# Performance work log

Measured on AMD Instinct MI355X. Metric: run time of the kernel, lower is better.

Reference implementation:

```python
import math
import jax, jax.numpy as jnp
import numpy as np

B, S, HID, NH = 4, 1024, 768, 12
D = HID // NH
R_ACT = 0.5
R_ATTN = 0.5


def act_prune_mask(a, ratio):
    # per-sample kth-smallest magnitude threshold (torch.kthvalue on flatten(1))
    n = int(np.prod(a.shape[1:]))
    k = int(np.clip(n * ratio, 1, n))
    mag = jnp.abs(a)
    thr = jnp.sort(mag.reshape(a.shape[0], -1), axis=1)[:, k - 1]
    thr = thr.reshape((a.shape[0],) + (1,) * (a.ndim - 1))
    return mag >= thr


def setup_inputs() -> dict:
    key = jax.random.key(0)
    ks = jax.random.split(key, 5)
    inp = {
        "hidden_states": jax.random.normal(ks[0], (B, S, HID), dtype=jnp.float32),
        "Wq": jax.random.normal(ks[1], (HID, HID), dtype=jnp.float32) * 0.02,
        "bq": jnp.zeros((HID,), dtype=jnp.float32),
        "Wk": jax.random.normal(ks[2], (HID, HID), dtype=jnp.float32) * 0.02,
        "bk": jnp.zeros((HID,), dtype=jnp.float32),
        "Wv": jax.random.normal(ks[3], (HID, HID), dtype=jnp.float32) * 0.02,
        "bv": jnp.zeros((HID,), dtype=jnp.float32),
        "Wo": jax.random.normal(ks[4], (HID, HID), dtype=jnp.float32) * 0.02,
        "bo": jnp.zeros((HID,), dtype=jnp.float32),
    }
    return inp


def reference(hidden_states, Wq, bq, Wk, bk, Wv, bv, Wo, bo):
    b, s, hid = hidden_states.shape

    # prune mask on input activations (saved for backward in the original; forward math unchanged)
    mask_h = act_prune_mask(hidden_states, R_ACT)
    _hs_prune = jnp.where(mask_h, hidden_states, 0.0)

    q = jnp.matmul(hidden_states, Wq.T) + bq
    k = jnp.matmul(hidden_states, Wk.T) + bk
    v = jnp.matmul(hidden_states, Wv.T) + bv

    def split_heads(x):
        return x.reshape(b, s, NH, D).transpose(0, 2, 1, 3)  # [B,H,S,D]

    q4, k4, v4 = split_heads(q), split_heads(k), split_heads(v)

    mask_q = act_prune_mask(q4, R_ACT)
    mask_k = act_prune_mask(k4, R_ACT)
    _qp = jnp.where(mask_q, q4, 0.0)
    _kp = jnp.where(mask_k, k4, 0.0)

    scores = jnp.einsum("bhqd,bhkd->bhqk", q4, k4) / math.sqrt(D)
    probs = jax.nn.softmax(scores, axis=-1)

    mask_p = act_prune_mask(probs, R_ATTN)
    _pp = jnp.where(mask_p, probs, 0.0)
    mask_v = act_prune_mask(v4, R_ACT)
    _vp = jnp.where(mask_v, v4, 0.0)

    ctx = jnp.einsum("bhqk,bhkd->bhqd", probs, v4)
    ctx = ctx.transpose(0, 2, 1, 3).reshape(b, s, hid)

    mask_c = act_prune_mask(ctx, R_ACT)
    _cp = jnp.where(mask_c, ctx, 0.0)

    out = jnp.matmul(ctx, Wo.T) + bo  # proj_dropout rate = 0.0 (identity)
    return (out, probs)  # vis=True -> weights = attention_probs
```

## Files before the change

kernel.cpp:

```cpp
#include <hip/hip_runtime.h>
#include <hip/hip_bf16.h>

typedef __attribute__((ext_vector_type(4))) float f32x4;
typedef __attribute__((ext_vector_type(8))) short bf16x8;
typedef __attribute__((ext_vector_type(4))) int i32x4;

#define SEQ 1024
#define HIDV 768
#define NH 12
#define HD 64
#define QBLK 64

static __device__ __forceinline__ unsigned short f2b(float f) {
  unsigned u = __builtin_bit_cast(unsigned, f);
  u = (u + 0x7fffu + ((u >> 16) & 1u)) >> 16;
  return (unsigned short)u;
}

static __device__ __forceinline__ void gl16(const unsigned short* g, unsigned short* l) {
  __builtin_amdgcn_global_load_lds(
      (const __attribute__((address_space(1))) unsigned int*)g,
      (__attribute__((address_space(3))) unsigned int*)l, 16, 0, 0);
}

static __device__ __forceinline__ void bar_lgkm() {
  asm volatile("s_waitcnt lgkmcnt(0)" ::: "memory");
  __builtin_amdgcn_sched_barrier(0);
  __builtin_amdgcn_s_barrier();
  __builtin_amdgcn_sched_barrier(0);
}

__global__ __launch_bounds__(256) void convert_all(
    const float* __restrict__ X, const float* __restrict__ Wq,
    const float* __restrict__ Wk, const float* __restrict__ Wv,
    const float* __restrict__ Wo, unsigned short* __restrict__ dst) {
  long i = (long)blockIdx.x * 256 + threadIdx.x;
  const long N4 = (3145728L + 4 * 589824L) / 4;
  if (i >= N4) return;
  long e = i * 4;
  const float* src; long off;
  if (e < 3145728L)      { src = X;  off = e; }
  else if (e < 3735552L) { src = Wq; off = e - 3145728L; }
  else if (e < 4325376L) { src = Wk; off = e - 3735552L; }
  else if (e < 4915200L) { src = Wv; off = e - 4325376L; }
  else                   { src = Wo; off = e - 4915200L; }
  const float4 v = *reinterpret_cast<const float4*>(src + off);
  ushort4 o;
  o.x = f2b(v.x); o.y = f2b(v.y); o.z = f2b(v.z); o.w = f2b(v.w);
  *reinterpret_cast<ushort4*>(dst + e) = o;
}

__global__ __launch_bounds__(256) void qkv_gemm(
    const unsigned short* __restrict__ Xb,
    const unsigned short* __restrict__ Wqb, const unsigned short* __restrict__ Wkb,
    const unsigned short* __restrict__ Wvb,
    const float* __restrict__ bq, const float* __restrict__ bk, const float* __restrict__ bv,
    unsigned short* __restrict__ Qh, unsigned short* __restrict__ Kh,
    unsigned short* __restrict__ VT) {
  __shared__ __align__(16) unsigned short la[2][128 * 32];
  __shared__ __align__(16) unsigned short lb[2][128 * 32];
  const int z = blockIdx.z;
  const unsigned short* Wb = (z == 0) ? Wqb : (z == 1) ? Wkb : Wvb;
  const float* bias = (z == 0) ? bq : (z == 1) ? bk : bv;
  const int m0 = blockIdx.x * 128, n0 = blockIdx.y * 128;
  const int tid = threadIdx.x;
  const int wave = tid >> 6, lane = tid & 63, g = lane >> 4, c = lane & 15;
  const int wr = (wave >> 1) * 64, wc = (wave & 1) * 64;

  const int sr = wave * 16 + (lane >> 2);
  const int scol = (lane & 3) * 8;
  const unsigned short* Ag = &Xb[(size_t)(m0 + sr) * HIDV + scol];
  const unsigned short* Bg = &Wb[(size_t)(n0 + sr) * HIDV + scol];

  gl16(Ag, &la[0][(wave * 16) * 32]);
  gl16(Ag + (size_t)64 * HIDV, &la[0][(64 + wave * 16) * 32]);
  gl16(Bg, &lb[0][(wave * 16) * 32]);
  gl16(Bg + (size_t)64 * HIDV, &lb[0][(64 + wave * 16) * 32]);
  __syncthreads();

  f32x4 acc[4][4] = {};
  for (int t = 0; t < 24; t++) {
    const int cur = t & 1;
    if (t < 23) {
      const int kt = (t + 1) * 32;
      gl16(Ag + kt, &la[cur ^ 1][(wave * 16) * 32]);
      gl16(Ag + (size_t)64 * HIDV + kt, &la[cur ^ 1][(64 + wave * 16) * 32]);
      gl16(Bg + kt, &lb[cur ^ 1][(wave * 16) * 32]);
      gl16(Bg + (size_t)64 * HIDV + kt, &lb[cur ^ 1][(64 + wave * 16) * 32]);
    }
    bf16x8 af[4], bfr[4];
#pragma unroll
    for (int m = 0; m < 4; m++)
      af[m] = *reinterpret_cast<bf16x8*>(&la[cur][(wr + m * 16 + c) * 32 + g * 8]);
#pragma unroll
    for (int n = 0; n < 4; n++)
      bfr[n] = *reinterpret_cast<bf16x8*>(&lb[cur][(wc + n * 16 + c) * 32 + g * 8]);
#pragma unroll
    for (int m = 0; m < 4; m++)
#pragma unroll
      for (int n = 0; n < 4; n++)
        acc[m][n] = __builtin_amdgcn_mfma_f32_16x16x32_bf16(af[m], bfr[n], acc[m][n], 0, 0, 0);
    __syncthreads();
  }
  float bv4[4];
#pragma unroll
  for (int n = 0; n < 4; n++) bv4[n] = bias[n0 + wc + n * 16 + c];
  if (z < 2) {
    unsigned short* dst = (z == 0) ? Qh : Kh;
#pragma unroll
    for (int m = 0; m < 4; m++) {
      int rb_ = m0 + wr + m * 16 + g * 4;
#pragma unroll
      for (int n = 0; n < 4; n++) {
        int col = n0 + wc + n * 16 + c;
        int h = col >> 6, d = col & 63;
#pragma unroll
        for (int r = 0; r < 4; r++) {
          int row = rb_ + r;
          int b = row >> 10, s = row & 1023;
          dst[((size_t)(b * NH + h) * SEQ + s) * HD + d] = f2b(acc[m][n][r] + bv4[n]);
        }
      }
    }
  } else {
#pragma unroll
    for (int m = 0; m < 4; m++) {
      int rb_ = m0 + wr + m * 16 + g * 4;
      int b = rb_ >> 10, s = rb_ & 1023;
#pragma unroll
      for (int n = 0; n < 4; n++) {
        int col = n0 + wc + n * 16 + c;
        int h = col >> 6, d = col & 63;
        ushort4 o;
        o.x = f2b(acc[m][n][0] + bv4[n]);
        o.y = f2b(acc[m][n][1] + bv4[n]);
        o.z = f2b(acc[m][n][2] + bv4[n]);
        o.w = f2b(acc[m][n][3] + bv4[n]);
        *reinterpret_cast<ushort4*>(&VT[((size_t)(b * NH + h) * HD + d) * SEQ + s]) = o;
      }
    }
  }
}

#define EXPC 0.18033688f
__global__ __launch_bounds__(256) void attn_fused(
    const unsigned short* __restrict__ Qh, const unsigned short* __restrict__ Kh,
    const unsigned short* __restrict__ VT,
    float* __restrict__ probs, unsigned short* __restrict__ CTX) {
  __shared__ __align__(16) unsigned short ldsk[2][64 * 72];
  __shared__ __align__(16) unsigned short ldsv[2][64 * 72];
  __shared__ __align__(16) unsigned short lp[64 * 72];
  const int lin = blockIdx.x;
  const int swz = (lin & 7) * 96 + (lin >> 3);
  const int bh = swz >> 4, rb = (swz & 15) * QBLK;
  const int b = bh / NH, h = bh - b * NH;
  const unsigned short* Qp = Qh + (size_t)bh * SEQ * HD;
  const unsigned short* Kp = Kh + (size_t)bh * SEQ * HD;
  const unsigned short* Vp = VT + (size_t)bh * HD * SEQ;
  float* P = probs + (size_t)bh * SEQ * SEQ;
  const int tid = threadIdx.x, wave = tid >> 6, lane = tid & 63, g = lane >> 4, c = lane & 15;
  const int wrow = wave * 16;
  const int str = tid >> 3;
  const int stc = (tid & 7) * 8;

  bf16x8 aq[2];
#pragma unroll
  for (int ks = 0; ks < 2; ks++)
    aq[ks] = *reinterpret_cast<const bf16x8*>(&Qp[(size_t)(rb + wrow + c) * HD + ks * 32 + g * 8]);

  i32x4 kr0, kr1, vr0, vr1;
  kr0 = *reinterpret_cast<const i32x4*>(&Kp[(size_t)str * HD + stc]);
  kr1 = *reinterpret_cast<const i32x4*>(&Kp[(size_t)(str + 32) * HD + stc]);
  *reinterpret_cast<i32x4*>(&ldsk[0][str * 72 + stc]) = kr0;
  *reinterpret_cast<i32x4*>(&ldsk[0][(str + 32) * 72 + stc]) = kr1;
  bar_lgkm();

  float lsum = 0.f;
  for (int ct = 0; ct < 16; ct++) {
    const int cur = ct & 1;
    if (ct < 15) {
      kr0 = *reinterpret_cast<const i32x4*>(&Kp[(size_t)((ct + 1) * 64 + str) * HD + stc]);
      kr1 = *reinterpret_cast<const i32x4*>(&Kp[(size_t)((ct + 1) * 64 + str + 32) * HD + stc]);
    }
    f32x4 sreg[4] = {};
    __builtin_amdgcn_s_setprio(1);
#pragma unroll
    for (int ks = 0; ks < 2; ks++) {
      bf16x8 kf[4];
#pragma unroll
      for (int kb = 0; kb < 4; kb++)
        kf[kb] = *reinterpret_cast<bf16x8*>(&ldsk[cur][(kb * 16 + c) * 72 + ks * 32 + g * 8]);
#pragma unroll
      for (int kb = 0; kb < 4; kb++)
        sreg[kb] = __builtin_amdgcn_mfma_f32_16x16x32_bf16(kf[kb], aq[ks], sreg[kb], 0, 0, 0);
    }
    __builtin_amdgcn_s_setprio(0);
#pragma unroll
    for (int kb = 0; kb < 4; kb++)
#pragma unroll
      for (int r = 0; r < 4; r++)
        lsum += __builtin_amdgcn_exp2f(sreg[kb][r] * EXPC);
    if (ct < 15) {
      *reinterpret_cast<i32x4*>(&ldsk[cur ^ 1][str * 72 + stc]) = kr0;
      *reinterpret_cast<i32x4*>(&ldsk[cur ^ 1][(str + 32) * 72 + stc]) = kr1;
      bar_lgkm();
    }
  }
  float s = lsum;
  s += __shfl_xor(s, 16);
  s += __shfl_xor(s, 32);
  const float linv = 1.f / s;

  kr0 = *reinterpret_cast<const i32x4*>(&Kp[(size_t)str * HD + stc]);
  kr1 = *reinterpret_cast<const i32x4*>(&Kp[(size_t)(str + 32) * HD + stc]);
  vr0 = *reinterpret_cast<const i32x4*>(&Vp[(size_t)str * SEQ + stc]);
  vr1 = *reinterpret_cast<const i32x4*>(&Vp[(size_t)(str + 32) * SEQ + stc]);
  *reinterpret_cast<i32x4*>(&ldsk[0][str * 72 + stc]) = kr0;
  *reinterpret_cast<i32x4*>(&ldsk[0][(str + 32) * 72 + stc]) = kr1;
  *reinterpret_cast<i32x4*>(&ldsv[0][str * 72 + stc]) = vr0;
  *reinterpret_cast<i32x4*>(&ldsv[0][(str + 32) * 72 + stc]) = vr1;
  bar_lgkm();

  f32x4 acc[4] = {};
  for (int ct = 0; ct < 16; ct++) {
    const int cur = ct & 1;
    if (ct < 15) {
      kr0 = *reinterpret_cast<const i32x4*>(&Kp[(size_t)((ct + 1) * 64 + str) * HD + stc]);
      kr1 = *reinterpret_cast<const i32x4*>(&Kp[(size_t)((ct + 1) * 64 + str + 32) * HD + stc]);
      vr0 = *reinterpret_cast<const i32x4*>(&Vp[(size_t)str * SEQ + (ct + 1) * 64 + stc]);
      vr1 = *reinterpret_cast<const i32x4*>(&Vp[(size_t)(str + 32) * SEQ + (ct + 1) * 64 + stc]);
    }
    f32x4 sreg[4] = {};
    __builtin_amdgcn_s_setprio(1);
#pragma unroll
    for (int ks = 0; ks < 2; ks++) {
      bf16x8 kf[4];
#pragma unroll
      for (int kb = 0; kb < 4; kb++)
        kf[kb] = *reinterpret_cast<bf16x8*>(&ldsk[cur][(kb * 16 + c) * 72 + ks * 32 + g * 8]);
#pragma unroll
      for (int kb = 0; kb < 4; kb++)
        sreg[kb] = __builtin_amdgcn_mfma_f32_16x16x32_bf16(kf[kb], aq[ks], sreg[kb], 0, 0, 0);
    }
    __builtin_amdgcn_s_setprio(0);
    {
      float* Prow = &P[(size_t)(rb + wrow + c) * SEQ + ct * 64];
#pragma unroll
      for (int kb = 0; kb < 4; kb++) {
        f32x4 p;
#pragma unroll
        for (int r = 0; r < 4; r++)
          p[r] = __builtin_amdgcn_exp2f(sreg[kb][r] * EXPC) * linv;
        *reinterpret_cast<f32x4*>(&Prow[kb * 16 + g * 4]) = p;
        uint2 pk;
        pk.x = (unsigned)f2b(p[0]) | ((unsigned)f2b(p[1]) << 16);
        pk.y = (unsigned)f2b(p[2]) | ((unsigned)f2b(p[3]) << 16);
        *reinterpret_cast<uint2*>(&lp[(wrow + c) * 72 + kb * 16 + g * 4]) = pk;
      }
    }
    __builtin_amdgcn_s_setprio(1);
#pragma unroll
    for (int ks = 0; ks < 2; ks++) {
      bf16x8 pa, vf[4];
      pa = *reinterpret_cast<bf16x8*>(&lp[(wrow + c) * 72 + ks * 32 + g * 8]);
#pragma unroll
      for (int db = 0; db < 4; db++)
        vf[db] = *reinterpret_cast<bf16x8*>(&ldsv[cur][(db * 16 + c) * 72 + ks * 32 + g * 8]);
#pragma unroll
      for (int db = 0; db < 4; db++)
        acc[db] = __builtin_amdgcn_mfma_f32_16x16x32_bf16(pa, vf[db], acc[db], 0, 0, 0);
    }
    __builtin_amdgcn_s_setprio(0);
    if (ct < 15) {
      *reinterpret_cast<i32x4*>(&ldsk[cur ^ 1][str * 72 + stc]) = kr0;
      *reinterpret_cast<i32x4*>(&ldsk[cur ^ 1][(str + 32) * 72 + stc]) = kr1;
      *reinterpret_cast<i32x4*>(&ldsv[cur ^ 1][str * 72 + stc]) = vr0;
      *reinterpret_cast<i32x4*>(&ldsv[cur ^ 1][(str + 32) * 72 + stc]) = vr1;
      bar_lgkm();
    }
  }

  bar_lgkm();
#pragma unroll
  for (int db = 0; db < 4; db++)
#pragma unroll
    for (int r = 0; r < 4; r++)
      lp[(wrow + g * 4 + r) * 72 + db * 16 + c] = f2b(acc[db][r]);
  bar_lgkm();
  {
    const int q = tid >> 2, seg = (tid & 3) * 16;
    const unsigned short* src = &lp[q * 72 + seg];
    unsigned short* dst = &CTX[(size_t)(b * SEQ + rb + q) * HIDV + h * HD + seg];
    i32x4 t0 = *reinterpret_cast<const i32x4*>(&src[0]);
    i32x4 t1 = *reinterpret_cast<const i32x4*>(&src[8]);
    *reinterpret_cast<i32x4*>(&dst[0]) = t0;
    *reinterpret_cast<i32x4*>(&dst[8]) = t1;
  }
}

__global__ __launch_bounds__(256) void proj_gemm(
    const unsigned short* __restrict__ Ab, const unsigned short* __restrict__ Wb,
    const float* __restrict__ bias, float* __restrict__ out) {
  __shared__ __align__(16) unsigned short la[2][64 * 32];
  __shared__ __align__(16) unsigned short lb[2][128 * 32];
  const int m0 = blockIdx.x * 64, n0 = blockIdx.y * 128;
  const int tid = threadIdx.x;
  const int wave = tid >> 6, lane = tid & 63, g = lane >> 4, c = lane & 15;
  const int wr = (wave >> 1) * 32, wc = (wave & 1) * 64;
  const int srb = wave * 16 + (lane >> 2);
  const int scol = (lane & 3) * 8;
  const unsigned short* Ag = &Ab[(size_t)(m0 + srb) * HIDV + scol];
  const unsigned short* Bg = &Wb[(size_t)(n0 + srb) * HIDV + scol];

#define PROJ_STAGE(buf, kt)                                               \
  do {                                                                    \
    gl16(Ag + (kt), &la[buf][(wave * 16) * 32]);                          \
    gl16(Bg + (kt), &lb[buf][(wave * 16) * 32]);                          \
    gl16(Bg + (size_t)64 * HIDV + (kt), &lb[buf][(64 + wave * 16) * 32]); \
  } while (0)

  PROJ_STAGE(0, 0);
  __syncthreads();

  f32x4 acc[2][4] = {};
  for (int t = 0; t < 24; t++) {
    const int cur = t & 1;
    if (t < 23) PROJ_STAGE(cur ^ 1, (t + 1) * 32);
    bf16x8 af[2], bfr[4];
#pragma unroll
    for (int m = 0; m < 2; m++)
      af[m] = *reinterpret_cast<bf16x8*>(&la[cur][(wr + m * 16 + c) * 32 + g * 8]);
#pragma unroll
    for (int n = 0; n < 4; n++)
      bfr[n] = *reinterpret_cast<bf16x8*>(&lb[cur][(wc + n * 16 + c) * 32 + g * 8]);
#pragma unroll
    for (int m = 0; m < 2; m++)
#pragma unroll
      for (int n = 0; n < 4; n++)
        acc[m][n] = __builtin_amdgcn_mfma_f32_16x16x32_bf16(af[m], bfr[n], acc[m][n], 0, 0, 0);
    __syncthreads();
  }
#undef PROJ_STAGE
  float bv4[4];
#pragma unroll
  for (int n = 0; n < 4; n++) bv4[n] = bias[n0 + wc + n * 16 + c];
#pragma unroll
  for (int m = 0; m < 2; m++) {
    int rb_ = m0 + wr + m * 16 + g * 4;
#pragma unroll
    for (int n = 0; n < 4; n++) {
      int col = n0 + wc + n * 16 + c;
#pragma unroll
      for (int r = 0; r < 4; r++)
        out[(size_t)(rb_ + r) * HIDV + col] = acc[m][n][r] + bv4[n];
    }
  }
}

extern "C" void kernel_launch(void* const* d_in, const int* in_sizes, int n_in,
                              void* d_out, int out_size, void* d_ws, size_t ws_size,
                              hipStream_t stream) {
  const float* X  = (const float*)d_in[0];
  const float* Wq = (const float*)d_in[1];
  const float* bq = (const float*)d_in[2];
  const float* Wk = (const float*)d_in[3];
  const float* bk = (const float*)d_in[4];
  const float* Wv = (const float*)d_in[5];
  const float* bv = (const float*)d_in[6];
  const float* Wo = (const float*)d_in[7];
  const float* bo = (const float*)d_in[8];
  float* out = (float*)d_out;
  float* probs = out + 3145728;

  unsigned short* Xb  = (unsigned short*)d_ws;
  unsigned short* Wqb = Xb + 3145728;
  unsigned short* Wkb = Wqb + 589824;
  unsigned short* Wvb = Wkb + 589824;
  unsigned short* Wob = Wvb + 589824;
  unsigned short* Qh  = Wob + 589824;
  unsigned short* Kh  = Qh + 3145728;
  unsigned short* VT  = Kh + 3145728;
  unsigned short* CTX = VT + 3145728;

  convert_all<<<5376, 256, 0, stream>>>(X, Wq, Wk, Wv, Wo, Xb);
  qkv_gemm<<<dim3(32, 6, 3), 256, 0, stream>>>(Xb, Wqb, Wkb, Wvb, bq, bk, bv, Qh, Kh, VT);
  attn_fused<<<dim3(768), 256, 0, stream>>>(Qh, Kh, VT, probs, CTX);
  proj_gemm<<<dim3(64, 6), 256, 0, stream>>>(CTX, Wob, bo, out);
}
```

Before: 105.8 us.

## Make attention single-pass by staging unnormalized bf16 exp scores in LDS

The attention kernel no longer runs a separate QK^T pass just to compute softmax row sums. It computes exp scores once and keeps them unnormalized as bf16 in a large dynamic LDS buffer covering the full 64x1024 score tile. It accumulates row sums alongside, then scales both the context output and the stored scores by 1/sum, writing probs to global memory in coalesced rows at the end. In exchange, LDS use grows to roughly 150 KB per block, K/V staging loses its double buffering, and probs are now rounded through bf16 before being written as fp32.

Result: slower. 165.5 us (+56.3%).

```diff
diff --git a/kernel.cpp b/kernel.cpp
--- a/kernel.cpp
+++ b/kernel.cpp
@@ -10,12 +10,17 @@
 #define NH 12
 #define HD 64
 #define QBLK 64
+#define SPITCH 1032
+#define ATTN_LDS ((64 * SPITCH + 2 * 64 * 72) * 2)
 
 static __device__ __forceinline__ unsigned short f2b(float f) {
   unsigned u = __builtin_bit_cast(unsigned, f);
   u = (u + 0x7fffu + ((u >> 16) & 1u)) >> 16;
   return (unsigned short)u;
 }
+static __device__ __forceinline__ float b2f(unsigned short u) {
+  return __builtin_bit_cast(float, (unsigned)u << 16);
+}
 
 static __device__ __forceinline__ void gl16(const unsigned short* g, unsigned short* l) {
   __builtin_amdgcn_global_load_lds(
@@ -25,6 +30,11 @@
 
 static __device__ __forceinline__ void bar_lgkm() {
   asm volatile("s_waitcnt lgkmcnt(0)" ::: "memory");
+  __builtin_amdgcn_sched_barrier(0);
+  __builtin_amdgcn_s_barrier();
+  __builtin_amdgcn_sched_barrier(0);
+}
+static __device__ __forceinline__ void bar_only() {
   __builtin_amdgcn_sched_barrier(0);
   __builtin_amdgcn_s_barrier();
   __builtin_amdgcn_sched_barrier(0);
@@ -147,9 +157,12 @@
     const unsigned short* __restrict__ Qh, const unsigned short* __restrict__ Kh,
     const unsigned short* __restrict__ VT,
     float* __restrict__ probs, unsigned short* __restrict__ CTX) {
-  __shared__ __align__(16) unsigned short ldsk[2][64 * 72];
-  __shared__ __align__(16) unsigned short ldsv[2][64 * 72];
-  __shared__ __align__(16) unsigned short lp[64 * 72];
+  extern __shared__ __align__(16) unsigned short smem[];
+  unsigned short* Sbuf = smem;
+  unsigned short* ldsk = smem + 64 * SPITCH;
+  unsigned short* ldsv = ldsk + 64 * 72;
+  float* linvf = (float*)ldsv;
+
   const int lin = blockIdx.x;
   const int swz = (lin & 7) * 96 + (lin >> 3);
   const int bh = swz >> 4, rb = (swz & 15) * QBLK;
@@ -171,59 +184,17 @@
   i32x4 kr0, kr1, vr0, vr1;
   kr0 = *reinterpret_cast<const i32x4*>(&Kp[(size_t)str * HD + stc]);
   kr1 = *reinterpret_cast<const i32x4*>(&Kp[(size_t)(str + 32) * HD + stc]);
-  *reinterpret_cast<i32x4*>(&ldsk[0][str * 72 + stc]) = kr0;
-  *reinterpret_cast<i32x4*>(&ldsk[0][(str + 32) * 72 + stc]) = kr1;
-  bar_lgkm();
-
-  float lsum = 0.f;
-  for (int ct = 0; ct < 16; ct++) {
-    const int cur = ct & 1;
-    if (ct < 15) {
-      kr0 = *reinterpret_cast<const i32x4*>(&Kp[(size_t)((ct + 1) * 64 + str) * HD + stc]);
-      kr1 = *reinterpret_cast<const i32x4*>(&Kp[(size_t)((ct + 1) * 64 + str + 32) * HD + stc]);
-    }
-    f32x4 sreg[4] = {};
-    __builtin_amdgcn_s_setprio(1);
-#pragma unroll
-    for (int ks = 0; ks < 2; ks++) {
-      bf16x8 kf[4];
-#pragma unroll
-      for (int kb = 0; kb < 4; kb++)
-        kf[kb] = *reinterpret_cast<bf16x8*>(&ldsk[cur][(kb * 16 + c) * 72 + ks * 32 + g * 8]);
-#pragma unroll
-      for (int kb = 0; kb < 4; kb++)
-        sreg[kb] = __builtin_amdgcn_mfma_f32_16x16x32_bf16(kf[kb], aq[ks], sreg[kb], 0, 0, 0);
-    }
-    __builtin_amdgcn_s_setprio(0);
-#pragma unroll
-    for (int kb = 0; kb < 4; kb++)
-#pragma unroll
-      for (int r = 0; r < 4; r++)
-        lsum += __builtin_amdgcn_exp2f(sreg[kb][r] * EXPC);
-    if (ct < 15) {
-      *reinterpret_cast<i32x4*>(&ldsk[cur ^ 1][str * 72 + stc]) = kr0;
-      *reinterpret_cast<i32x4*>(&ldsk[cur ^ 1][(str + 32) * 72 + stc]) = kr1;
-      bar_lgkm();
-    }
-  }
-  float s = lsum;
-  s += __shfl_xor(s, 16);
-  s += __shfl_xor(s, 32);
-  const float linv = 1.f / s;
-
-  kr0 = *reinterpret_cast<const i32x4*>(&Kp[(size_t)str * HD + stc]);
-  kr1 = *reinterpret_cast<const i32x4*>(&Kp[(size_t)(str + 32) * HD + stc]);
   vr0 = *reinterpret_cast<const i32x4*>(&Vp[(size_t)str * SEQ + stc]);
   vr1 = *reinterpret_cast<const i32x4*>(&Vp[(size_t)(str + 32) * SEQ + stc]);
-  *reinterpret_cast<i32x4*>(&ldsk[0][str * 72 + stc]) = kr0;
-  *reinterpret_cast<i32x4*>(&ldsk[0][(str + 32) * 72 + stc]) = kr1;
-  *reinterpret_cast<i32x4*>(&ldsv[0][str * 72 + stc]) = vr0;
-  *reinterpret_cast<i32x4*>(&ldsv[0][(str + 32) * 72 + stc]) = vr1;
+  *reinterpret_cast<i32x4*>(&ldsk[str * 72 + stc]) = kr0;
+  *reinterpret_cast<i32x4*>(&ldsk[(str + 32) * 72 + stc]) = kr1;
+  *reinterpret_cast<i32x4*>(&ldsv[str * 72 + stc]) = vr0;
+  *reinterpret_cast<i32x4*>(&ldsv[(str + 32) * 72 + stc]) = vr1;
   bar_lgkm();
 
+  float lsum = 0.f;
   f32x4 acc[4] = {};
   for (int ct = 0; ct < 16; ct++) {
-    const int cur = ct & 1;
     if (ct < 15) {
       kr0 = *reinterpret_cast<const i32x4*>(&Kp[(size_t)((ct + 1) * 64 + str) * HD + stc]);
       kr1 = *reinterpret_cast<const i32x4*>(&Kp[(size_t)((ct + 1) * 64 + str + 32) * HD + stc]);
@@ -237,64 +208,87 @@
       bf16x8 kf[4];
 #pragma unroll
       for (int kb = 0; kb < 4; kb++)
-        kf[kb] = *reinterpret_cast<bf16x8*>(&ldsk[cur][(kb * 16 + c) * 72 + ks * 32 + g * 8]);
+        kf[kb] = *reinterpret_cast<bf16x8*>(&ldsk[(kb * 16 + c) * 72 + ks * 32 + g * 8]);
 #pragma unroll
       for (int kb = 0; kb < 4; kb++)
         sreg[kb] = __builtin_amdgcn_mfma_f32_16x16x32_bf16(kf[kb], aq[ks], sreg[kb], 0, 0, 0);
     }
     __builtin_amdgcn_s_setprio(0);
     {
-      float* Prow = &P[(size_t)(rb + wrow + c) * SEQ + ct * 64];
+      unsigned short* srow = &Sbuf[(wrow + c) * SPITCH + ct * 64];
 #pragma unroll
       for (int kb = 0; kb < 4; kb++) {
         f32x4 p;
 #pragma unroll
-        for (int r = 0; r < 4; r++)
-          p[r] = __builtin_amdgcn_exp2f(sreg[kb][r] * EXPC) * linv;
-        *reinterpret_cast<f32x4*>(&Prow[kb * 16 + g * 4]) = p;
+        for (int r = 0; r < 4; r++) {
+          p[r] = __builtin_amdgcn_exp2f(sreg[kb][r] * EXPC);
+          lsum += p[r];
+        }
         uint2 pk;
         pk.x = (unsigned)f2b(p[0]) | ((unsigned)f2b(p[1]) << 16);
         pk.y = (unsigned)f2b(p[2]) | ((unsigned)f2b(p[3]) << 16);
-        *reinterpret_cast<uint2*>(&lp[(wrow + c) * 72 + kb * 16 + g * 4]) = pk;
+        *reinterpret_cast<uint2*>(&srow[kb * 16 + g * 4]) = pk;
       }
     }
     __builtin_amdgcn_s_setprio(1);
 #pragma unroll
     for (int ks = 0; ks < 2; ks++) {
       bf16x8 pa, vf[4];
-      pa = *reinterpret_cast<bf16x8*>(&lp[(wrow + c) * 72 + ks * 32 + g * 8]);
+      pa = *reinterpret_cast<bf16x8*>(&Sbuf[(wrow + c) * SPITCH + ct * 64 + ks * 32 + g * 8]);
 #pragma unroll
       for (int db = 0; db < 4; db++)
-        vf[db] = *reinterpret_cast<bf16x8*>(&ldsv[cur][(db * 16 + c) * 72 + ks * 32 + g * 8]);
+        vf[db] = *reinterpret_cast<bf16x8*>(&ldsv[(db * 16 + c) * 72 + ks * 32 + g * 8]);
 #pragma unroll
       for (int db = 0; db < 4; db++)
         acc[db] = __builtin_amdgcn_mfma_f32_16x16x32_bf16(pa, vf[db], acc[db], 0, 0, 0);
     }
     __builtin_amdgcn_s_setprio(0);
     if (ct < 15) {
-      *reinterpret_cast<i32x4*>(&ldsk[cur ^ 1][str * 72 + stc]) = kr0;
-      *reinterpret_cast<i32x4*>(&ldsk[cur ^ 1][(str + 32) * 72 + stc]) = kr1;
-      *reinterpret_cast<i32x4*>(&ldsv[cur ^ 1][str * 72 + stc]) = vr0;
-      *reinterpret_cast<i32x4*>(&ldsv[cur ^ 1][(str + 32) * 72 + stc]) = vr1;
+      bar_only();
+      *reinterpret_cast<i32x4*>(&ldsk[str * 72 + stc]) = kr0;
+      *reinterpret_cast<i32x4*>(&ldsk[(str + 32) * 72 + stc]) = kr1;
+      *reinterpret_cast<i32x4*>(&ldsv[str * 72 + stc]) = vr0;
+      *reinterpret_cast<i32x4*>(&ldsv[(str + 32) * 72 + stc]) = vr1;
       bar_lgkm();
     }
   }
 
-  bar_lgkm();
+  float s = lsum;
+  s += __shfl_xor(s, 16);
+  s += __shfl_xor(s, 32);
+  const float linv = 1.f / s;
+  bar_only();
+  if (lane < 16) linvf[wrow + lane] = linv;
+
+  float lv[4];
+#pragma unroll
+  for (int r = 0; r < 4; r++) lv[r] = linvf[wrow + g * 4 + r];
 #pragma unroll
   for (int db = 0; db < 4; db++)
 #pragma unroll
     for (int r = 0; r < 4; r++)
-      lp[(wrow + g * 4 + r) * 72 + db * 16 + c] = f2b(acc[db][r]);
+      ldsk[(wrow + g * 4 + r) * 72 + db * 16 + c] = f2b(acc[db][r] * lv[r]);
   bar_lgkm();
   {
     const int q = tid >> 2, seg = (tid & 3) * 16;
-    const unsigned short* src = &lp[q * 72 + seg];
+    const unsigned short* src = &ldsk[q * 72 + seg];
     unsigned short* dst = &CTX[(size_t)(b * SEQ + rb + q) * HIDV + h * HD + seg];
     i32x4 t0 = *reinterpret_cast<const i32x4*>(&src[0]);
     i32x4 t1 = *reinterpret_cast<const i32x4*>(&src[8]);
     *reinterpret_cast<i32x4*>(&dst[0]) = t0;
     *reinterpret_cast<i32x4*>(&dst[8]) = t1;
+  }
+
+#pragma unroll 4
+  for (int r = 0; r < 64; r++) {
+    const float lr = linvf[r];
+    uint2 pk = *reinterpret_cast<const uint2*>(&Sbuf[r * SPITCH + tid * 4]);
+    float4 o;
+    o.x = b2f((unsigned short)(pk.x & 0xffff)) * lr;
+    o.y = b2f((unsigned short)(pk.x >> 16)) * lr;
+    o.z = b2f((unsigned short)(pk.y & 0xffff)) * lr;
+    o.w = b2f((unsigned short)(pk.y >> 16)) * lr;
+    *reinterpret_cast<float4*>(&P[(size_t)(rb + r) * SEQ + tid * 4]) = o;
   }
 }
 
@@ -382,8 +376,11 @@
   unsigned short* VT  = Kh + 3145728;
   unsigned short* CTX = VT + 3145728;
 
+  hipFuncSetAttribute(reinterpret_cast<const void*>(attn_fused),
+                      hipFuncAttributeMaxDynamicSharedMemorySize, ATTN_LDS);
+
   convert_all<<<5376, 256, 0, stream>>>(X, Wq, Wk, Wv, Wo, Xb);
   qkv_gemm<<<dim3(32, 6, 3), 256, 0, stream>>>(Xb, Wqb, Wkb, Wvb, bq, bk, bv, Qh, Kh, VT);
-  attn_fused<<<dim3(768), 256, 0, stream>>>(Qh, Kh, VT, probs, CTX);
+  attn_fused<<<dim3(768), 256, ATTN_LDS, stream>>>(Qh, Kh, VT, probs, CTX);
   proj_gemm<<<dim3(64, 6), 256, 0, stream>>>(CTX, Wob, bo, out);
 }
```

## Fuse two-pass softmax into single pass with deferred normalization of probs and context

Applied to the files above, without the earlier changes.

Removes the first pass over K that computed the softmax denominator, and instead accumulates the row sum during the single QK/PV pass using unnormalized exponentials. The unnormalized probabilities are kept in registers as packed bf16 (64 uint2 per thread), then scaled by the inverse sum and written to the fp32 probs output at the end; the context accumulator is rescaled per row before the store. This halves the QK^T matmul work and K traffic, but raises register pressure considerably and makes the stored probs bf16-rounded values. There is no running max subtraction, matching the prior code.

Measured after the change: 148.2 us. 40.0% more time.

```diff
diff --git a/kernel.cpp b/kernel.cpp
--- a/kernel.cpp
+++ b/kernel.cpp
@@ -15,6 +15,9 @@
   unsigned u = __builtin_bit_cast(unsigned, f);
   u = (u + 0x7fffu + ((u >> 16) & 1u)) >> 16;
   return (unsigned short)u;
+}
+static __device__ __forceinline__ float b2f(unsigned short u) {
+  return __builtin_bit_cast(float, (unsigned)u << 16);
 }
 
 static __device__ __forceinline__ void gl16(const unsigned short* g, unsigned short* l) {
@@ -171,48 +174,6 @@
   i32x4 kr0, kr1, vr0, vr1;
   kr0 = *reinterpret_cast<const i32x4*>(&Kp[(size_t)str * HD + stc]);
   kr1 = *reinterpret_cast<const i32x4*>(&Kp[(size_t)(str + 32) * HD + stc]);
-  *reinterpret_cast<i32x4*>(&ldsk[0][str * 72 + stc]) = kr0;
-  *reinterpret_cast<i32x4*>(&ldsk[0][(str + 32) * 72 + stc]) = kr1;
-  bar_lgkm();
-
-  float lsum = 0.f;
-  for (int ct = 0; ct < 16; ct++) {
-    const int cur = ct & 1;
-    if (ct < 15) {
-      kr0 = *reinterpret_cast<const i32x4*>(&Kp[(size_t)((ct + 1) * 64 + str) * HD + stc]);
-      kr1 = *reinterpret_cast<const i32x4*>(&Kp[(size_t)((ct + 1) * 64 + str + 32) * HD + stc]);
-    }
-    f32x4 sreg[4] = {};
-    __builtin_amdgcn_s_setprio(1);
-#pragma unroll
-    for (int ks = 0; ks < 2; ks++) {
-      bf16x8 kf[4];
-#pragma unroll
-      for (int kb = 0; kb < 4; kb++)
-        kf[kb] = *reinterpret_cast<bf16x8*>(&ldsk[cur][(kb * 16 + c) * 72 + ks * 32 + g * 8]);
-#pragma unroll
-      for (int kb = 0; kb < 4; kb++)
-        sreg[kb] = __builtin_amdgcn_mfma_f32_16x16x32_bf16(kf[kb], aq[ks], sreg[kb], 0, 0, 0);
-    }
-    __builtin_amdgcn_s_setprio(0);
-#pragma unroll
-    for (int kb = 0; kb < 4; kb++)
-#pragma unroll
-      for (int r = 0; r < 4; r++)
-        lsum += __builtin_amdgcn_exp2f(sreg[kb][r] * EXPC);
-    if (ct < 15) {
-      *reinterpret_cast<i32x4*>(&ldsk[cur ^ 1][str * 72 + stc]) = kr0;
-      *reinterpret_cast<i32x4*>(&ldsk[cur ^ 1][(str + 32) * 72 + stc]) = kr1;
-      bar_lgkm();
-    }
-  }
-  float s = lsum;
-  s += __shfl_xor(s, 16);
-  s += __shfl_xor(s, 32);
-  const float linv = 1.f / s;
-
-  kr0 = *reinterpret_cast<const i32x4*>(&Kp[(size_t)str * HD + stc]);
-  kr1 = *reinterpret_cast<const i32x4*>(&Kp[(size_t)(str + 32) * HD + stc]);
   vr0 = *reinterpret_cast<const i32x4*>(&Vp[(size_t)str * SEQ + stc]);
   vr1 = *reinterpret_cast<const i32x4*>(&Vp[(size_t)(str + 32) * SEQ + stc]);
   *reinterpret_cast<i32x4*>(&ldsk[0][str * 72 + stc]) = kr0;
@@ -221,7 +182,10 @@
   *reinterpret_cast<i32x4*>(&ldsv[0][(str + 32) * 72 + stc]) = vr1;
   bar_lgkm();
 
+  uint2 pst[16][4];
+  float lsum = 0.f;
   f32x4 acc[4] = {};
+#pragma unroll
   for (int ct = 0; ct < 16; ct++) {
     const int cur = ct & 1;
     if (ct < 15) {
@@ -244,17 +208,18 @@
     }
     __builtin_amdgcn_s_setprio(0);
     {
-      float* Prow = &P[(size_t)(rb + wrow + c) * SEQ + ct * 64];
 #pragma unroll
       for (int kb = 0; kb < 4; kb++) {
         f32x4 p;
 #pragma unroll
-        for (int r = 0; r < 4; r++)
-          p[r] = __builtin_amdgcn_exp2f(sreg[kb][r] * EXPC) * linv;
-        *reinterpret_cast<f32x4*>(&Prow[kb * 16 + g * 4]) = p;
+        for (int r = 0; r < 4; r++) {
+          p[r] = __builtin_amdgcn_exp2f(sreg[kb][r] * EXPC);
+          lsum += p[r];
+        }
         uint2 pk;
         pk.x = (unsigned)f2b(p[0]) | ((unsigned)f2b(p[1]) << 16);
         pk.y = (unsigned)f2b(p[2]) | ((unsigned)f2b(p[3]) << 16);
+        pst[ct][kb] = pk;
         *reinterpret_cast<uint2*>(&lp[(wrow + c) * 72 + kb * 16 + g * 4]) = pk;
       }
     }
@@ -280,12 +245,36 @@
     }
   }
 
+  float s = lsum;
+  s += __shfl_xor(s, 16);
+  s += __shfl_xor(s, 32);
+  const float linv = 1.f / s;
+
+  {
+    float* Prow = &P[(size_t)(rb + wrow + c) * SEQ];
+#pragma unroll
+    for (int ct = 0; ct < 16; ct++)
+#pragma unroll
+      for (int kb = 0; kb < 4; kb++) {
+        uint2 pk = pst[ct][kb];
+        float4 o;
+        o.x = b2f((unsigned short)(pk.x & 0xffff)) * linv;
+        o.y = b2f((unsigned short)(pk.x >> 16)) * linv;
+        o.z = b2f((unsigned short)(pk.y & 0xffff)) * linv;
+        o.w = b2f((unsigned short)(pk.y >> 16)) * linv;
+        *reinterpret_cast<float4*>(&Prow[ct * 64 + kb * 16 + g * 4]) = o;
+      }
+  }
+
+  float lvr[4];
+#pragma unroll
+  for (int r = 0; r < 4; r++) lvr[r] = __shfl(linv, g * 4 + r);
   bar_lgkm();
 #pragma unroll
   for (int db = 0; db < 4; db++)
 #pragma unroll
     for (int r = 0; r < 4; r++)
-      lp[(wrow + g * 4 + r) * 72 + db * 16 + c] = f2b(acc[db][r]);
+      lp[(wrow + g * 4 + r) * 72 + db * 16 + c] = f2b(acc[db][r] * lvr[r]);
   bar_lgkm();
   {
     const int q = tid >> 2, seg = (tid & 3) * 16;
```
